# Kernel tuning notes

Measured on AMD Instinct MI355X. Metric: run time of the kernel, lower is better.

The kernel has to match this reference:

```python
import jax, jax.numpy as jnp
import numpy as np
from jax import lax

NUM_HEADS = 4
EPS = 1e-12  # torch F.normalize eps


def _conv1x1(x, w):
    # x: [b, cin, h, w], w: [cout, cin] -> [b, cout, h, w]
    return jnp.einsum('bchw,oc->bohw', x, w)


def _dwconv3x3(x, w):
    # depthwise 3x3, padding=1; w: [C, 1, 3, 3]
    return lax.conv_general_dilated(
        x, w, window_strides=(1, 1), padding='SAME',
        feature_group_count=x.shape[1],
        dimension_numbers=('NCHW', 'OIHW', 'NCHW'))


def _l2norm(x):
    # F.normalize over last dim
    n = jnp.linalg.norm(x, axis=-1, keepdims=True)
    return x / jnp.maximum(n, EPS)


def _mdta(q, k, v, temperature, h, w):
    # q,k,v: [b, C, h, w] -> channel attention per head -> [b, C, h, w]
    b, c, _, _ = q.shape
    ch = c // NUM_HEADS
    def to_heads(t):
        return t.reshape(b, NUM_HEADS, ch, h * w)  # b head c (hw)
    qh, kh, vh = to_heads(q), to_heads(k), to_heads(v)
    qh = _l2norm(qh)
    kh = _l2norm(kh)
    attn = jnp.einsum('bhcn,bhdn->bhcd', qh, kh) * temperature  # [b,head,ch,ch]
    attn = jax.nn.softmax(attn, axis=-1)
    out = jnp.einsum('bhcd,bhdn->bhcn', attn, vh)
    return out.reshape(b, c, h, w)


def setup_inputs() -> dict:
    key = jax.random.key(0)
    ks = jax.random.split(key, 7)
    b, c, h, w = 2, 192, 128, 128
    return {
        'x': jax.random.normal(ks[0], (b, c, h, w), jnp.float32),
        'y': jax.random.normal(ks[1], (b, c, h, w), jnp.float32),
        'qkv_w': jax.random.normal(ks[2], (3 * c, c), jnp.float32) * (1.0 / np.sqrt(c)),
        'dw_w': jax.random.normal(ks[3], (3 * c, 1, 3, 3), jnp.float32) * (1.0 / 3.0),
        'kv_w': jax.random.normal(ks[4], (2 * c, c), jnp.float32) * (1.0 / np.sqrt(c)),
        'proj_w': jax.random.normal(ks[5], (c, c), jnp.float32) * (1.0 / np.sqrt(c)),
        'temperature': jnp.ones((NUM_HEADS, 1, 1), jnp.float32),
    }


def reference(x, y, qkv_w, dw_w, kv_w, proj_w, temperature):
    b, c, h, w = x.shape
    qkv = _dwconv3x3(_conv1x1(x, qkv_w), dw_w)
    q, k, v = jnp.split(qkv, 3, axis=1)
    # intra_fusion_attention(q, y): kv from y, channel attention with q
    kv = _conv1x1(y, kv_w)
    k2, v2 = jnp.split(kv, 2, axis=1)
    q = _mdta(q, k2, v2, temperature, h, w)
    out = _mdta(q, k, v, temperature, h, w)
    return _conv1x1(out, proj_w)
```

## Files before the change

kernel.cpp:

```cpp
#include <hip/hip_runtime.h>
#include <hip/hip_bf16.h>

#define HW 16384
#define IMGW 128
#define Bsz 2
#define Cc 192
#define NH 4
#define CH 48
static const size_t CP = (size_t)Cc * HW;

typedef __attribute__((ext_vector_type(4))) float f32x4;
typedef __attribute__((ext_vector_type(8))) short short8;
typedef __attribute__((ext_vector_type(8))) unsigned short bf16x8;
typedef __attribute__((ext_vector_type(4))) unsigned short bf16x4;

__device__ __forceinline__ unsigned short f2bf(float f) {
  __hip_bfloat16 h = __float2bfloat16(f);
  return *reinterpret_cast<unsigned short*>(&h);
}
__device__ __forceinline__ float bf2f(unsigned short u) {
  union { unsigned int i; float f; } v;
  v.i = (unsigned int)u << 16;
  return v.f;
}

#define NWQKV (576 * 192)
#define NWKV  (384 * 192)
__global__ __launch_bounds__(256) void cast_weights_kernel(
    const float* __restrict__ qkv_w, const float* __restrict__ kv_w,
    unsigned short* __restrict__ wqkv, unsigned short* __restrict__ wkv) {
  int i = blockIdx.x * 256 + threadIdx.x;
  if (i < NWQKV) wqkv[i] = f2bf(qkv_w[i]);
  else if (i < NWQKV + NWKV) wkv[i - NWQKV] = f2bf(kv_w[i - NWQKV]);
}

#define APAD 200

template <int INKIND, int OUTBF16>
__global__ __launch_bounds__(256) void conv_mfma_kernel(
    const void* __restrict__ src, size_t src_bstride,
    const unsigned short* __restrict__ wb, size_t wstride,
    void* __restrict__ outv, int Cout) {
  __shared__ __align__(16) short As[64 * APAD];
  __shared__ __align__(16) short Bs[64 * APAD];
  unsigned int* As32 = (unsigned int*)As;
  const int b = blockIdx.z;
  const int hw0 = blockIdx.x * 64;
  const int tid = threadIdx.x;
  const int lane = tid & 63, wid = tid >> 6;
  const int wm = wid & 1, wn = wid >> 1;
  const int l = tid & 15, pp0 = tid >> 4;
  const unsigned short* wbbase = wb + (size_t)b * wstride;
  const int NT = Cout >> 6;

  #pragma unroll
  for (int kp = 0; kp < 3; ++kp) {
    #pragma unroll
    for (int it = 0; it < 2; ++it) {
      int pp = pp0 + 16 * it;
      int c0 = kp * 64 + 2 * pp;
      if (INKIND == 1) {
        const float* r0 = (const float*)src + (size_t)b * src_bstride +
                          (size_t)c0 * HW + hw0 + l * 4;
        f32x4 v0 = *(const f32x4*)r0;
        f32x4 v1 = *(const f32x4*)(r0 + HW);
        #pragma unroll
        for (int i = 0; i < 4; ++i)
          As32[(l * 4 + i) * (APAD / 2) + kp * 32 + pp] =
              (unsigned int)f2bf(v0[i]) | ((unsigned int)f2bf(v1[i]) << 16);
      } else {
        const unsigned short* r0 = (const unsigned short*)src +
                                   (size_t)b * src_bstride +
                                   (size_t)c0 * HW + hw0 + l * 4;
        bf16x4 v0 = *(const bf16x4*)r0;
        bf16x4 v1 = *(const bf16x4*)(r0 + HW);
        #pragma unroll
        for (int i = 0; i < 4; ++i)
          As32[(l * 4 + i) * (APAD / 2) + kp * 32 + pp] =
              (unsigned int)v0[i] | ((unsigned int)v1[i] << 16);
      }
    }
  }

  for (int ot = 0; ot < NT; ++ot) {
    const unsigned short* wbb = wbbase + (size_t)(ot * 64) * Cc;
    #pragma unroll
    for (int p = 0; p < 6; ++p) {
      int i = tid + p * 256;
      int row = i / 24, cc = i - (i / 24) * 24;
      *(short8*)&Bs[row * APAD + cc * 8] =
          *(const short8*)(wbb + (size_t)row * Cc + cc * 8);
    }
    __syncthreads();
    f32x4 acc[2][2] = {};
    #pragma unroll
    for (int ks = 0; ks < 6; ++ks) {
      short8 bfrag[2];
      #pragma unroll
      for (int fn = 0; fn < 2; ++fn)
        bfrag[fn] = *(short8*)&Bs[(wn * 32 + fn * 16 + (lane & 15)) * APAD +
                                  ks * 32 + (lane >> 4) * 8];
      #pragma unroll
      for (int fm = 0; fm < 2; ++fm) {
        short8 afrag = *(short8*)&As[(wm * 32 + fm * 16 + (lane & 15)) * APAD +
                                     ks * 32 + (lane >> 4) * 8];
        #pragma unroll
        for (int fn = 0; fn < 2; ++fn)
          acc[fm][fn] = __builtin_amdgcn_mfma_f32_16x16x32_bf16(
              afrag, bfrag[fn], acc[fm][fn], 0, 0, 0);
      }
    }
    __syncthreads();
    #pragma unroll
    for (int fm = 0; fm < 2; ++fm)
      #pragma unroll
      for (int fn = 0; fn < 2; ++fn) {
        int o = ot * 64 + wn * 32 + fn * 16 + (lane & 15);
        int hw = hw0 + wm * 32 + fm * 16 + ((lane >> 4) << 2);
        if (OUTBF16) {
          bf16x4 u;
          #pragma unroll
          for (int r = 0; r < 4; ++r) u[r] = f2bf(acc[fm][fn][r]);
          *(bf16x4*)&((unsigned short*)outv)[((size_t)b * Cout + o) * HW + hw] = u;
        } else {
          *(f32x4*)&((float*)outv)[((size_t)b * Cout + o) * HW + hw] = acc[fm][fn];
        }
      }
  }
}

__global__ __launch_bounds__(256) void dwconv_kernel(
    const unsigned short* __restrict__ in, const float* __restrict__ wgt,
    unsigned short* __restrict__ out, int Ctot) {
  const int b = blockIdx.z, ch = blockIdx.y;
  const int p0 = blockIdx.x * 2048 + threadIdx.x * 8;
  const int y = p0 >> 7, x0 = p0 & 127;
  const unsigned short* ip = in + ((size_t)b * Ctot + ch) * HW;
  const float* wp = wgt + ch * 9;
  float acc[8] = {};
  #pragma unroll
  for (int dy = -1; dy <= 1; ++dy) {
    int yy = y + dy;
    if (yy < 0 || yy > IMGW - 1) continue;
    const unsigned short* rp = ip + yy * IMGW;
    float r[10];
    bf16x8 mid = *(const bf16x8*)&rp[x0];
    #pragma unroll
    for (int e = 0; e < 8; ++e) r[e + 1] = bf2f(mid[e]);
    r[0] = (x0 > 0) ? bf2f(rp[x0 - 1]) : 0.f;
    r[9] = (x0 < 120) ? bf2f(rp[x0 + 8]) : 0.f;
    #pragma unroll
    for (int dx = 0; dx < 3; ++dx) {
      float wv = wp[(dy + 1) * 3 + dx];
      #pragma unroll
      for (int e = 0; e < 8; ++e) acc[e] += wv * r[e + dx];
    }
  }
  bf16x8 u;
  #pragma unroll
  for (int e = 0; e < 8; ++e) u[e] = f2bf(acc[e]);
  *(bf16x8*)&out[((size_t)b * Ctot + ch) * HW + p0] = u;
}

#define PK 136
#define NCHUNK 16
__global__ __launch_bounds__(256) void gram_mfma_kernel(
    const unsigned short* __restrict__ qkvb,
    const unsigned short* __restrict__ kvb, float* __restrict__ spart,
    float* __restrict__ spartN) {
  __shared__ __align__(16) char lds_raw[4 * 2304 * 4];
  short* Qs = (short*)lds_raw;
  short* Ks = Qs + 48 * PK;
  float* Rs = (float*)lds_raw;
  const int pair = blockIdx.z;
  const int bh = blockIdx.y, b = bh >> 2, hd = bh & 3;
  const int n0 = blockIdx.x * 1024;
  const int tid = threadIdx.x, lane = tid & 63, wid = tid >> 6;
  const unsigned short *ap, *bp;
  size_t as_, bs_;
  if (pair == 0)      { ap = qkvb;      as_ = 3 * CP; bp = kvb;       bs_ = 2 * CP; }
  else if (pair == 1) { ap = kvb + CP;  as_ = 2 * CP; bp = qkvb + CP; bs_ = 3 * CP; }
  else                { ap = kvb + CP;  as_ = 2 * CP; bp = kvb + CP;  bs_ = 2 * CP; }
  const unsigned short* qb = ap + (size_t)b * as_ + (size_t)(hd * CH) * HW + n0;
  const unsigned short* kb = bp + (size_t)b * bs_ + (size_t)(hd * CH) * HW + n0;
  f32x4 acc[3][3] = {};
  float sqA[3] = {}, sqB[3] = {};
  #pragma unroll 1
  for (int it = 0; it < 8; ++it) {
    #pragma unroll
    for (int p = 0; p < 3; ++p) {
      int c = tid + p * 256;
      int row = c >> 4, col = c & 15;
      short8 vq = *(const short8*)(qb + (size_t)row * HW + it * 128 + col * 8);
      short8 vk = *(const short8*)(kb + (size_t)row * HW + it * 128 + col * 8);
      *(short8*)&Qs[row * PK + col * 8] = vq;
      *(short8*)&Ks[row * PK + col * 8] = vk;
      if (pair == 0) {
        float aq = 0.f, ak = 0.f;
        #pragma unroll
        for (int j = 0; j < 8; ++j) {
          float q = bf2f((unsigned short)vq[j]);
          float k = bf2f((unsigned short)vk[j]);
          aq += q * q;
          ak += k * k;
        }
        sqA[p] += aq;
        sqB[p] += ak;
      } else if (pair == 1) {
        float ak = 0.f;
        #pragma unroll
        for (int j = 0; j < 8; ++j) {
          float k = bf2f((unsigned short)vk[j]);
          ak += k * k;
        }
        sqB[p] += ak;
      }
    }
    __syncthreads();
    short8 af[3], bfr[3];
    #pragma unroll
    for (int t = 0; t < 3; ++t) {
      af[t]  = *(short8*)&Qs[(t * 16 + (lane & 15)) * PK + wid * 32 + (lane >> 4) * 8];
      bfr[t] = *(short8*)&Ks[(t * 16 + (lane & 15)) * PK + wid * 32 + (lane >> 4) * 8];
    }
    #pragma unroll
    for (int mt = 0; mt < 3; ++mt)
      #pragma unroll
      for (int nt = 0; nt < 3; ++nt)
        acc[mt][nt] = __builtin_amdgcn_mfma_f32_16x16x32_bf16(
            af[mt], bfr[nt], acc[mt][nt], 0, 0, 0);
    __syncthreads();
  }
  if (pair < 2) {
    #pragma unroll
    for (int p = 0; p < 3; ++p)
      #pragma unroll
      for (int off = 1; off < 16; off <<= 1) {
        if (pair == 0) sqA[p] += __shfl_xor(sqA[p], off);
        sqB[p] += __shfl_xor(sqB[p], off);
      }
    if ((tid & 15) == 0) {
      int r0 = tid >> 4;
      float* np = spartN + ((size_t)bh * NCHUNK + blockIdx.x) * 144;
      #pragma unroll
      for (int p = 0; p < 3; ++p) {
        if (pair == 0) {
          np[r0 + 16 * p] = sqA[p];
          np[48 + r0 + 16 * p] = sqB[p];
        } else {
          np[96 + r0 + 16 * p] = sqB[p];
        }
      }
    }
  }
  #pragma unroll
  for (int mt = 0; mt < 3; ++mt)
    #pragma unroll
    for (int nt = 0; nt < 3; ++nt)
      #pragma unroll
      for (int r = 0; r < 4; ++r) {
        int i = mt * 16 + ((lane >> 4) << 2) + r;
        int j = nt * 16 + (lane & 15);
        Rs[wid * 2304 + i * 48 + j] = acc[mt][nt][r];
      }
  __syncthreads();
  float* sp = spart + ((size_t)(pair * 8 + bh) * NCHUNK + blockIdx.x) * 2304;
  for (int e = tid; e < 2304; e += 256)
    sp[e] = Rs[e] + Rs[2304 + e] + Rs[2 * 2304 + e] + Rs[3 * 2304 + e];
}

__global__ __launch_bounds__(256) void reduce_kernel(
    const float* __restrict__ spart, const float* __restrict__ spartN,
    float* __restrict__ G, float* __restrict__ inv) {
  int idx = blockIdx.x * 256 + threadIdx.x;
  if (idx < 3 * 8 * 2304) {
    int pb = idx / 2304;
    int e = idx - pb * 2304;
    const float* sp = spart + (size_t)pb * NCHUNK * 2304 + e;
    float s = 0.f;
    #pragma unroll
    for (int c = 0; c < NCHUNK; ++c) s += sp[(size_t)c * 2304];
    G[idx] = s;
  } else if (idx < 3 * 8 * 2304 + 1152) {
    int t = idx - 3 * 8 * 2304;
    int kind = t / 384;
    int row = t - kind * 384;
    int b = row / 192;
    int rr = row - b * 192;
    int hd = rr / 48, r = rr - hd * 48;
    int bh = b * 4 + hd;
    const float* np = spartN + (size_t)bh * NCHUNK * 144 + kind * 48 + r;
    float s = 0.f;
    #pragma unroll
    for (int c = 0; c < NCHUNK; ++c) s += np[c * 144];
    inv[t] = 1.f / fmaxf(sqrtf(s), 1e-12f);
  }
}

__global__ __launch_bounds__(256) void finalize_kernel(
    const float* __restrict__ G, const float* __restrict__ inv,
    const float* __restrict__ temp, const float* __restrict__ proj_w,
    unsigned short* __restrict__ Mb) {
  __shared__ float A1[2304], GVV[2304], GVK[2304], S2[2304];
  __shared__ unsigned short Pb[192 * 48];
  __shared__ float invq1[48];
  const int bh = blockIdx.x, b = bh >> 2, hd = bh & 3;
  const int tid = threadIdx.x;
  const float tp = temp[hd];
  const float* invQ  = inv;
  const float* invK2 = inv + 384;
  const float* invK  = inv + 768;
  for (int e = tid; e < 192 * 48; e += 256) {
    int o = e / 48, i = e - (e / 48) * 48;
    Pb[e] = f2bf(proj_w[(size_t)o * Cc + hd * 48 + i]);
  }
  for (int e = tid; e < 2304; e += 256) {
    int i = e / 48, j = e - i * 48;
    A1[e] = G[(size_t)(0 * 8 + bh) * 2304 + e] *
            invQ[b * Cc + hd * CH + i] * invK2[b * Cc + hd * CH + j] * tp;
    GVV[e] = G[(size_t)(2 * 8 + bh) * 2304 + e];
    GVK[e] = G[(size_t)(1 * 8 + bh) * 2304 + e];
  }
  __syncthreads();
  if (tid < 192) {
    const int i = tid >> 2, g = tid & 3;
    float v[12];
    float m = -1e30f;
    #pragma unroll
    for (int k = 0; k < 12; ++k) {
      v[k] = A1[i * 48 + g * 12 + k];
      m = fmaxf(m, v[k]);
    }
    m = fmaxf(m, __shfl_xor(m, 1));
    m = fmaxf(m, __shfl_xor(m, 2));
    float sum = 0.f;
    #pragma unroll
    for (int k = 0; k < 12; ++k) {
      v[k] = expf(v[k] - m);
      sum += v[k];
    }
    sum += __shfl_xor(sum, 1);
    sum += __shfl_xor(sum, 2);
    float r = 1.f / sum;
    #pragma unroll
    for (int k = 0; k < 12; ++k) A1[i * 48 + g * 12 + k] = v[k] * r;
  }
  __syncthreads();
  const int ti = tid >> 4, tj = tid & 15;
  {
    float c[3][3] = {};
    #pragma unroll 4
    for (int d = 0; d < 48; ++d) {
      float a0 = A1[ti * 48 + d], a1 = A1[(ti + 16) * 48 + d],
            a2 = A1[(ti + 32) * 48 + d];
      float b0 = GVV[d * 48 + tj], b1 = GVV[d * 48 + tj + 16],
            b2 = GVV[d * 48 + tj + 32];
      c[0][0] += a0 * b0; c[0][1] += a0 * b1; c[0][2] += a0 * b2;
      c[1][0] += a1 * b0; c[1][1] += a1 * b1; c[1][2] += a1 * b2;
      c[2][0] += a2 * b0; c[2][1] += a2 * b1; c[2][2] += a2 * b2;
    }
    #pragma unroll
    for (int ii = 0; ii < 3; ++ii) {
      float p = 0.f;
      #pragma unroll
      for (int jj = 0; jj < 3; ++jj)
        p += c[ii][jj] * A1[(ti + 16 * ii) * 48 + tj + 16 * jj];
      p += __shfl_xor(p, 1);
      p += __shfl_xor(p, 2);
      p += __shfl_xor(p, 4);
      p += __shfl_xor(p, 8);
      if (tj == 0)
        invq1[ti + 16 * ii] = 1.f / fmaxf(sqrtf(fmaxf(p, 0.f)), 1e-12f);
    }
  }
  __syncthreads();
  {
    float s[3][3] = {};
    #pragma unroll 4
    for (int d = 0; d < 48; ++d) {
      float a0 = A1[ti * 48 + d], a1 = A1[(ti + 16) * 48 + d],
            a2 = A1[(ti + 32) * 48 + d];
      float b0 = GVK[d * 48 + tj], b1 = GVK[d * 48 + tj + 16],
            b2 = GVK[d * 48 + tj + 32];
      s[0][0] += a0 * b0; s[0][1] += a0 * b1; s[0][2] += a0 * b2;
      s[1][0] += a1 * b0; s[1][1] += a1 * b1; s[1][2] += a1 * b2;
      s[2][0] += a2 * b0; s[2][1] += a2 * b1; s[2][2] += a2 * b2;
    }
    #pragma unroll
    for (int ii = 0; ii < 3; ++ii)
      #pragma unroll
      for (int jj = 0; jj < 3; ++jj) {
        int i = ti + 16 * ii, j = tj + 16 * jj;
        S2[i * 48 + j] = s[ii][jj] * invq1[i] *
                         invK[b * Cc + hd * CH + j] * tp;
      }
  }
  __syncthreads();
  if (tid < 192) {
    const int i = tid >> 2, g = tid & 3;
    float v[12];
    float m = -1e30f;
    #pragma unroll
    for (int k = 0; k < 12; ++k) {
      v[k] = S2[i * 48 + g * 12 + k];
      m = fmaxf(m, v[k]);
    }
    m = fmaxf(m, __shfl_xor(m, 1));
    m = fmaxf(m, __shfl_xor(m, 2));
    float sum = 0.f;
    #pragma unroll
    for (int k = 0; k < 12; ++k) {
      v[k] = expf(v[k] - m);
      sum += v[k];
    }
    sum += __shfl_xor(sum, 1);
    sum += __shfl_xor(sum, 2);
    float r = 1.f / sum;
    #pragma unroll
    for (int k = 0; k < 12; ++k) S2[i * 48 + g * 12 + k] = v[k] * r;
  }
  __syncthreads();
  {
    float macc[12][3] = {};
    #pragma unroll 4
    for (int d = 0; d < 48; ++d) {
      float b0 = S2[d * 48 + tj], b1 = S2[d * 48 + tj + 16],
            b2 = S2[d * 48 + tj + 32];
      #pragma unroll
      for (int rr = 0; rr < 12; ++rr) {
        float a = bf2f(Pb[(rr * 16 + ti) * 48 + d]);
        macc[rr][0] += a * b0;
        macc[rr][1] += a * b1;
        macc[rr][2] += a * b2;
      }
    }
    #pragma unroll
    for (int rr = 0; rr < 12; ++rr)
      #pragma unroll
      for (int cc = 0; cc < 3; ++cc) {
        int o = rr * 16 + ti, j = tj + 16 * cc;
        Mb[((size_t)b * Cc + o) * Cc + hd * 48 + j] = f2bf(macc[rr][cc]);
      }
  }
}

extern "C" void kernel_launch(void* const* d_in, const int* in_sizes, int n_in,
                              void* d_out, int out_size, void* d_ws, size_t ws_size,
                              hipStream_t stream) {
  const float* x      = (const float*)d_in[0];
  const float* y      = (const float*)d_in[1];
  const float* qkv_w  = (const float*)d_in[2];
  const float* dw_w   = (const float*)d_in[3];
  const float* kv_w   = (const float*)d_in[4];
  const float* proj_w = (const float*)d_in[5];
  const float* temp   = (const float*)d_in[6];
  float* out = (float*)d_out;
  float* ws  = (float*)d_ws;

  const size_t SF = (size_t)Bsz * CP;
  unsigned short* qkvb   = (unsigned short*)ws;
  unsigned short* kvb    = (unsigned short*)(ws + 3 * SF / 2);
  unsigned short* qkvpre = (unsigned short*)(ws + 5 * SF / 2);
  float* inv    = ws + 4 * SF;
  float* spart  = inv + 1152;
  float* spartN = spart + (size_t)3 * 8 * NCHUNK * 2304;
  float* G      = spartN + (size_t)8 * NCHUNK * 144;
  unsigned short* Mb   = (unsigned short*)(G + 3 * 8 * 2304);
  unsigned short* wqkv = Mb + (size_t)Bsz * Cc * Cc;
  unsigned short* wkv  = wqkv + NWQKV;

  dim3 blk(256);

  cast_weights_kernel<<<dim3((NWQKV + NWKV + 255) / 256), blk, 0, stream>>>(
      qkv_w, kv_w, wqkv, wkv);

  conv_mfma_kernel<1, 1><<<dim3(HW / 64, 1, Bsz), blk, 0, stream>>>(
      x, CP, wqkv, 0, qkvpre, 3 * Cc);
  dwconv_kernel<<<dim3(HW / 2048, 3 * Cc, Bsz), blk, 0, stream>>>(
      qkvpre, dw_w, qkvb, 3 * Cc);
  conv_mfma_kernel<1, 1><<<dim3(HW / 64, 1, Bsz), blk, 0, stream>>>(
      y, CP, wkv, 0, kvb, 2 * Cc);

  gram_mfma_kernel<<<dim3(NCHUNK, 8, 3), blk, 0, stream>>>(
      qkvb, kvb, spart, spartN);
  reduce_kernel<<<dim3((3 * 8 * 2304 + 1152 + 255) / 256), blk, 0, stream>>>(
      spart, spartN, G, inv);

  finalize_kernel<<<dim3(8), blk, 0, stream>>>(G, inv, temp, proj_w, Mb);

  conv_mfma_kernel<2, 0><<<dim3(HW / 64, 1, Bsz), blk, 0, stream>>>(
      qkvb + 2 * CP, 3 * CP, Mb, (size_t)Cc * Cc, out, Cc);
}
```

Baseline: 119.8 us.

## Fuse depthwise conv into gram and projection kernels, merge front convs

Removes the standalone depthwise 3x3 pass and recomputes the depthwise conv on the fly inside the gram kernel (for q and k) and inside the final projection GEMM's A-tile load (for v). The two front 1x1 convs become one launch, and the weight bf16 cast is folded into the B-tile loads, which drops the separate cast kernel. The aim is to avoid writing and re-reading the full qkv intermediate and to cut kernel launches. In exchange, the stencil is computed redundantly with extra halo loads, weights are re-converted per block, and a 3x9-float weight array adds register pressure in the gram kernel.

```diff
diff --git a/kernel.cpp b/kernel.cpp
--- a/kernel.cpp
+++ b/kernel.cpp
@@ -24,34 +24,80 @@
   return v.f;
 }
 
-#define NWQKV (576 * 192)
-#define NWKV  (384 * 192)
-__global__ __launch_bounds__(256) void cast_weights_kernel(
+__device__ __forceinline__ short8 dw3x3_row8(
+    const unsigned short* __restrict__ chimg, int yrow, int x0,
+    const float* __restrict__ w9) {
+  float acc[8] = {};
+  #pragma unroll
+  for (int dy = -1; dy <= 1; ++dy) {
+    int yy = yrow + dy;
+    if (yy >= 0 && yy <= IMGW - 1) {
+      const unsigned short* rp = chimg + yy * IMGW;
+      float r[10];
+      bf16x8 mid = *(const bf16x8*)&rp[x0];
+      #pragma unroll
+      for (int e = 0; e < 8; ++e) r[e + 1] = bf2f(mid[e]);
+      r[0] = (x0 > 0) ? bf2f(rp[x0 - 1]) : 0.f;
+      r[9] = (x0 < 120) ? bf2f(rp[x0 + 8]) : 0.f;
+      #pragma unroll
+      for (int dx = 0; dx < 3; ++dx) {
+        float wv = w9[(dy + 1) * 3 + dx];
+        #pragma unroll
+        for (int e = 0; e < 8; ++e) acc[e] += wv * r[e + dx];
+      }
+    }
+  }
+  short8 o;
+  #pragma unroll
+  for (int e = 0; e < 8; ++e) o[e] = (short)f2bf(acc[e]);
+  return o;
+}
+
+__device__ __forceinline__ void dw3x3_row4(
+    const unsigned short* __restrict__ chimg, const float* __restrict__ w9,
+    int yrow, int xb, float* __restrict__ acc) {
+  acc[0] = acc[1] = acc[2] = acc[3] = 0.f;
+  #pragma unroll
+  for (int dy = -1; dy <= 1; ++dy) {
+    int yy = yrow + dy;
+    if (yy >= 0 && yy <= IMGW - 1) {
+      const unsigned short* rp = chimg + yy * IMGW;
+      float r[6];
+      bf16x4 mid = *(const bf16x4*)&rp[xb];
+      #pragma unroll
+      for (int i = 0; i < 4; ++i) r[i + 1] = bf2f(mid[i]);
+      r[0] = (xb > 0) ? bf2f(rp[xb - 1]) : 0.f;
+      r[5] = (xb < 124) ? bf2f(rp[xb + 4]) : 0.f;
+      #pragma unroll
+      for (int dx = 0; dx < 3; ++dx) {
+        float wv = w9[(dy + 1) * 3 + dx];
+        #pragma unroll
+        for (int i = 0; i < 4; ++i) acc[i] += wv * r[i + dx];
+      }
+    }
+  }
+}
+
+#define APAD 200
+
+__global__ __launch_bounds__(256) void conv_front_kernel(
+    const float* __restrict__ xin, const float* __restrict__ yin,
     const float* __restrict__ qkv_w, const float* __restrict__ kv_w,
-    unsigned short* __restrict__ wqkv, unsigned short* __restrict__ wkv) {
-  int i = blockIdx.x * 256 + threadIdx.x;
-  if (i < NWQKV) wqkv[i] = f2bf(qkv_w[i]);
-  else if (i < NWQKV + NWKV) wkv[i - NWQKV] = f2bf(kv_w[i - NWQKV]);
-}
-
-#define APAD 200
-
-template <int INKIND, int OUTBF16>
-__global__ __launch_bounds__(256) void conv_mfma_kernel(
-    const void* __restrict__ src, size_t src_bstride,
-    const unsigned short* __restrict__ wb, size_t wstride,
-    void* __restrict__ outv, int Cout) {
+    unsigned short* __restrict__ qkvpre, unsigned short* __restrict__ kvb) {
   __shared__ __align__(16) short As[64 * APAD];
   __shared__ __align__(16) short Bs[64 * APAD];
   unsigned int* As32 = (unsigned int*)As;
-  const int b = blockIdx.z;
+  const int z = blockIdx.z, isKV = z >> 1, b = z & 1;
+  const float* src = isKV ? yin : xin;
+  const float* wsrc = isKV ? kv_w : qkv_w;
+  unsigned short* dst = isKV ? kvb : qkvpre;
+  const int Cout = isKV ? 2 * Cc : 3 * Cc;
+  const int NT = Cout >> 6;
   const int hw0 = blockIdx.x * 64;
   const int tid = threadIdx.x;
   const int lane = tid & 63, wid = tid >> 6;
   const int wm = wid & 1, wn = wid >> 1;
   const int l = tid & 15, pp0 = tid >> 4;
-  const unsigned short* wbbase = wb + (size_t)b * wstride;
-  const int NT = Cout >> 6;
 
   #pragma unroll
   for (int kp = 0; kp < 3; ++kp) {
@@ -59,37 +105,32 @@
     for (int it = 0; it < 2; ++it) {
       int pp = pp0 + 16 * it;
       int c0 = kp * 64 + 2 * pp;
-      if (INKIND == 1) {
-        const float* r0 = (const float*)src + (size_t)b * src_bstride +
-                          (size_t)c0 * HW + hw0 + l * 4;
-        f32x4 v0 = *(const f32x4*)r0;
-        f32x4 v1 = *(const f32x4*)(r0 + HW);
-        #pragma unroll
-        for (int i = 0; i < 4; ++i)
-          As32[(l * 4 + i) * (APAD / 2) + kp * 32 + pp] =
-              (unsigned int)f2bf(v0[i]) | ((unsigned int)f2bf(v1[i]) << 16);
-      } else {
-        const unsigned short* r0 = (const unsigned short*)src +
-                                   (size_t)b * src_bstride +
-                                   (size_t)c0 * HW + hw0 + l * 4;
-        bf16x4 v0 = *(const bf16x4*)r0;
-        bf16x4 v1 = *(const bf16x4*)(r0 + HW);
-        #pragma unroll
-        for (int i = 0; i < 4; ++i)
-          As32[(l * 4 + i) * (APAD / 2) + kp * 32 + pp] =
-              (unsigned int)v0[i] | ((unsigned int)v1[i] << 16);
-      }
+      const float* r0 = src + (size_t)b * CP + (size_t)c0 * HW + hw0 + l * 4;
+      f32x4 v0 = *(const f32x4*)r0;
+      f32x4 v1 = *(const f32x4*)(r0 + HW);
+      #pragma unroll
+      for (int i = 0; i < 4; ++i)
+        As32[(l * 4 + i) * (APAD / 2) + kp * 32 + pp] =
+            (unsigned int)f2bf(v0[i]) | ((unsigned int)f2bf(v1[i]) << 16);
     }
   }
 
   for (int ot = 0; ot < NT; ++ot) {
-    const unsigned short* wbb = wbbase + (size_t)(ot * 64) * Cc;
+    const float* wbb = wsrc + (size_t)(ot * 64) * Cc;
     #pragma unroll
     for (int p = 0; p < 6; ++p) {
       int i = tid + p * 256;
       int row = i / 24, cc = i - (i / 24) * 24;
-      *(short8*)&Bs[row * APAD + cc * 8] =
-          *(const short8*)(wbb + (size_t)row * Cc + cc * 8);
+      const float* wr = wbb + (size_t)row * Cc + cc * 8;
+      f32x4 w0 = *(const f32x4*)wr;
+      f32x4 w1 = *(const f32x4*)(wr + 4);
+      short8 v;
+      #pragma unroll
+      for (int j = 0; j < 4; ++j) {
+        v[j] = (short)f2bf(w0[j]);
+        v[j + 4] = (short)f2bf(w1[j]);
+      }
+      *(short8*)&Bs[row * APAD + cc * 8] = v;
     }
     __syncthreads();
     f32x4 acc[2][2] = {};
@@ -117,90 +158,88 @@
       for (int fn = 0; fn < 2; ++fn) {
         int o = ot * 64 + wn * 32 + fn * 16 + (lane & 15);
         int hw = hw0 + wm * 32 + fm * 16 + ((lane >> 4) << 2);
-        if (OUTBF16) {
-          bf16x4 u;
-          #pragma unroll
-          for (int r = 0; r < 4; ++r) u[r] = f2bf(acc[fm][fn][r]);
-          *(bf16x4*)&((unsigned short*)outv)[((size_t)b * Cout + o) * HW + hw] = u;
-        } else {
-          *(f32x4*)&((float*)outv)[((size_t)b * Cout + o) * HW + hw] = acc[fm][fn];
-        }
-      }
-  }
-}
-
-__global__ __launch_bounds__(256) void dwconv_kernel(
-    const unsigned short* __restrict__ in, const float* __restrict__ wgt,
-    unsigned short* __restrict__ out, int Ctot) {
-  const int b = blockIdx.z, ch = blockIdx.y;
-  const int p0 = blockIdx.x * 2048 + threadIdx.x * 8;
-  const int y = p0 >> 7, x0 = p0 & 127;
-  const unsigned short* ip = in + ((size_t)b * Ctot + ch) * HW;
-  const float* wp = wgt + ch * 9;
-  float acc[8] = {};
-  #pragma unroll
-  for (int dy = -1; dy <= 1; ++dy) {
-    int yy = y + dy;
-    if (yy < 0 || yy > IMGW - 1) continue;
-    const unsigned short* rp = ip + yy * IMGW;
-    float r[10];
-    bf16x8 mid = *(const bf16x8*)&rp[x0];
-    #pragma unroll
-    for (int e = 0; e < 8; ++e) r[e + 1] = bf2f(mid[e]);
-    r[0] = (x0 > 0) ? bf2f(rp[x0 - 1]) : 0.f;
-    r[9] = (x0 < 120) ? bf2f(rp[x0 + 8]) : 0.f;
-    #pragma unroll
-    for (int dx = 0; dx < 3; ++dx) {
-      float wv = wp[(dy + 1) * 3 + dx];
-      #pragma unroll
-      for (int e = 0; e < 8; ++e) acc[e] += wv * r[e + dx];
-    }
-  }
-  bf16x8 u;
-  #pragma unroll
-  for (int e = 0; e < 8; ++e) u[e] = f2bf(acc[e]);
-  *(bf16x8*)&out[((size_t)b * Ctot + ch) * HW + p0] = u;
+        bf16x4 u;
+        #pragma unroll
+        for (int r = 0; r < 4; ++r) u[r] = f2bf(acc[fm][fn][r]);
+        *(bf16x4*)&dst[((size_t)b * Cout + o) * HW + hw] = u;
+      }
+  }
 }
 
 #define PK 136
 #define NCHUNK 16
 __global__ __launch_bounds__(256) void gram_mfma_kernel(
-    const unsigned short* __restrict__ qkvb,
-    const unsigned short* __restrict__ kvb, float* __restrict__ spart,
-    float* __restrict__ spartN) {
+    const unsigned short* __restrict__ qkvpre,
+    const unsigned short* __restrict__ kvb,
+    const float* __restrict__ dw_w,
+    float* __restrict__ spart, float* __restrict__ spartN) {
   __shared__ __align__(16) char lds_raw[4 * 2304 * 4];
   short* Qs = (short*)lds_raw;
   short* Ks = Qs + 48 * PK;
   float* Rs = (float*)lds_raw;
   const int pair = blockIdx.z;
   const int bh = blockIdx.y, b = bh >> 2, hd = bh & 3;
-  const int n0 = blockIdx.x * 1024;
+  const int chunk = blockIdx.x;
+  const int n0 = chunk * 1024;
   const int tid = threadIdx.x, lane = tid & 63, wid = tid >> 6;
-  const unsigned short *ap, *bp;
-  size_t as_, bs_;
-  if (pair == 0)      { ap = qkvb;      as_ = 3 * CP; bp = kvb;       bs_ = 2 * CP; }
-  else if (pair == 1) { ap = kvb + CP;  as_ = 2 * CP; bp = qkvb + CP; bs_ = 3 * CP; }
-  else                { ap = kvb + CP;  as_ = 2 * CP; bp = kvb + CP;  bs_ = 2 * CP; }
-  const unsigned short* qb = ap + (size_t)b * as_ + (size_t)(hd * CH) * HW + n0;
-  const unsigned short* kb = bp + (size_t)b * bs_ + (size_t)(hd * CH) * HW + n0;
+  const unsigned short* plainA = nullptr;
+  const unsigned short* plainB = nullptr;
+  const unsigned short* stA = nullptr;
+  const unsigned short* stB = nullptr;
+  const float* sW = nullptr;
+  if (pair == 0) {
+    stA = qkvpre + (size_t)b * 3 * CP;
+    sW = dw_w;
+    plainB = kvb + (size_t)b * 2 * CP;
+  } else if (pair == 1) {
+    plainA = kvb + (size_t)b * 2 * CP + CP;
+    stB = qkvpre + (size_t)b * 3 * CP + CP;
+    sW = dw_w + 192 * 9;
+  } else {
+    plainA = kvb + (size_t)b * 2 * CP + CP;
+    plainB = plainA;
+  }
+  int rowp[3];
+  #pragma unroll
+  for (int p = 0; p < 3; ++p) rowp[p] = (tid + p * 256) >> 4;
+  const int colx = (tid & 15) * 8;
+  float w9[3][9];
+  if (pair < 2) {
+    #pragma unroll
+    for (int p = 0; p < 3; ++p) {
+      const float* wp = sW + (size_t)(hd * CH + rowp[p]) * 9;
+      #pragma unroll
+      for (int k = 0; k < 9; ++k) w9[p][k] = wp[k];
+    }
+  }
   f32x4 acc[3][3] = {};
   float sqA[3] = {}, sqB[3] = {};
   #pragma unroll 1
   for (int it = 0; it < 8; ++it) {
+    const int yrow = chunk * 8 + it;
     #pragma unroll
     for (int p = 0; p < 3; ++p) {
-      int c = tid + p * 256;
-      int row = c >> 4, col = c & 15;
-      short8 vq = *(const short8*)(qb + (size_t)row * HW + it * 128 + col * 8);
-      short8 vk = *(const short8*)(kb + (size_t)row * HW + it * 128 + col * 8);
-      *(short8*)&Qs[row * PK + col * 8] = vq;
-      *(short8*)&Ks[row * PK + col * 8] = vk;
+      int row = rowp[p];
+      size_t choff = (size_t)(hd * CH + row) * HW;
+      short8 va, vb;
+      if (pair == 0) {
+        va = dw3x3_row8(stA + choff, yrow, colx, w9[p]);
+        vb = *(const short8*)(plainB + choff + n0 + it * 128 + colx);
+      } else if (pair == 1) {
+        va = *(const short8*)(plainA + choff + n0 + it * 128 + colx);
+        vb = dw3x3_row8(stB + choff, yrow, colx, w9[p]);
+      } else {
+        va = *(const short8*)(plainA + choff + n0 + it * 128 + colx);
+        vb = va;
+      }
+      *(short8*)&Qs[row * PK + colx] = va;
+      *(short8*)&Ks[row * PK + colx] = vb;
       if (pair == 0) {
         float aq = 0.f, ak = 0.f;
         #pragma unroll
         for (int j = 0; j < 8; ++j) {
-          float q = bf2f((unsigned short)vq[j]);
-          float k = bf2f((unsigned short)vk[j]);
+          float q = bf2f((unsigned short)va[j]);
+          float k = bf2f((unsigned short)vb[j]);
           aq += q * q;
           ak += k * k;
         }
@@ -210,7 +249,7 @@
         float ak = 0.f;
         #pragma unroll
         for (int j = 0; j < 8; ++j) {
-          float k = bf2f((unsigned short)vk[j]);
+          float k = bf2f((unsigned short)vb[j]);
           ak += k * k;
         }
         sqB[p] += ak;
@@ -241,7 +280,7 @@
       }
     if ((tid & 15) == 0) {
       int r0 = tid >> 4;
-      float* np = spartN + ((size_t)bh * NCHUNK + blockIdx.x) * 144;
+      float* np = spartN + ((size_t)bh * NCHUNK + chunk) * 144;
       #pragma unroll
       for (int p = 0; p < 3; ++p) {
         if (pair == 0) {
@@ -264,7 +303,7 @@
         Rs[wid * 2304 + i * 48 + j] = acc[mt][nt][r];
       }
   __syncthreads();
-  float* sp = spart + ((size_t)(pair * 8 + bh) * NCHUNK + blockIdx.x) * 2304;
+  float* sp = spart + ((size_t)(pair * 8 + bh) * NCHUNK + chunk) * 2304;
   for (int e = tid; e < 2304; e += 256)
     sp[e] = Rs[e] + Rs[2304 + e] + Rs[2 * 2304 + e] + Rs[3 * 2304 + e];
 }
@@ -444,6 +483,81 @@
   }
 }
 
+__global__ __launch_bounds__(256) void conv_back_kernel(
+    const unsigned short* __restrict__ qkvpre, const float* __restrict__ dw_w,
+    const unsigned short* __restrict__ Mb, float* __restrict__ out) {
+  __shared__ __align__(16) short As[64 * APAD];
+  __shared__ __align__(16) short Bs[64 * APAD];
+  unsigned int* As32 = (unsigned int*)As;
+  const int b = blockIdx.z;
+  const int hw0 = blockIdx.x * 64;
+  const int tid = threadIdx.x;
+  const int lane = tid & 63, wid = tid >> 6;
+  const int wm = wid & 1, wn = wid >> 1;
+  const int l = tid & 15, pp0 = tid >> 4;
+  const unsigned short* vbase = qkvpre + (size_t)b * 3 * CP + 2 * CP;
+  const float* dwv = dw_w + 384 * 9;
+  const unsigned short* wbbase = Mb + (size_t)b * Cc * Cc;
+  const int yimg = hw0 >> 7;
+  const int xb = (hw0 & 127) + l * 4;
+
+  #pragma unroll
+  for (int kp = 0; kp < 3; ++kp) {
+    #pragma unroll
+    for (int it = 0; it < 2; ++it) {
+      int pp = pp0 + 16 * it;
+      int c0 = kp * 64 + 2 * pp;
+      float a0[4], a1[4];
+      dw3x3_row4(vbase + (size_t)c0 * HW, dwv + (size_t)c0 * 9, yimg, xb, a0);
+      dw3x3_row4(vbase + (size_t)(c0 + 1) * HW, dwv + (size_t)(c0 + 1) * 9,
+                 yimg, xb, a1);
+      #pragma unroll
+      for (int i = 0; i < 4; ++i)
+        As32[(l * 4 + i) * (APAD / 2) + kp * 32 + pp] =
+            (unsigned int)f2bf(a0[i]) | ((unsigned int)f2bf(a1[i]) << 16);
+    }
+  }
+
+  for (int ot = 0; ot < 3; ++ot) {
+    const unsigned short* wbb = wbbase + (size_t)(ot * 64) * Cc;
+    #pragma unroll
+    for (int p = 0; p < 6; ++p) {
+      int i = tid + p * 256;
+      int row = i / 24, cc = i - (i / 24) * 24;
+      *(short8*)&Bs[row * APAD + cc * 8] =
+          *(const short8*)(wbb + (size_t)row * Cc + cc * 8);
+    }
+    __syncthreads();
+    f32x4 acc[2][2] = {};
+    #pragma unroll
+    for (int ks = 0; ks < 6; ++ks) {
+      short8 bfrag[2];
+      #pragma unroll
+      for (int fn = 0; fn < 2; ++fn)
+        bfrag[fn] = *(short8*)&Bs[(wn * 32 + fn * 16 + (lane & 15)) * APAD +
+                                  ks * 32 + (lane >> 4) * 8];
+      #pragma unroll
+      for (int fm = 0; fm < 2; ++fm) {
+        short8 afrag = *(short8*)&As[(wm * 32 + fm * 16 + (lane & 15)) * APAD +
+                                     ks * 32 + (lane >> 4) * 8];
+        #pragma unroll
+        for (int fn = 0; fn < 2; ++fn)
+          acc[fm][fn] = __builtin_amdgcn_mfma_f32_16x16x32_bf16(
+              afrag, bfrag[fn], acc[fm][fn], 0, 0, 0);
+      }
+    }
+    __syncthreads();
+    #pragma unroll
+    for (int fm = 0; fm < 2; ++fm)
+      #pragma unroll
+      for (int fn = 0; fn < 2; ++fn) {
+        int o = ot * 64 + wn * 32 + fn * 16 + (lane & 15);
+        int hw = hw0 + wm * 32 + fm * 16 + ((lane >> 4) << 2);
+        *(f32x4*)&out[((size_t)b * Cc + o) * HW + hw] = acc[fm][fn];
+      }
+  }
+}
+
 extern "C" void kernel_launch(void* const* d_in, const int* in_sizes, int n_in,
                               void* d_out, int out_size, void* d_ws, size_t ws_size,
                               hipStream_t stream) {
@@ -458,36 +572,27 @@
   float* ws  = (float*)d_ws;
 
   const size_t SF = (size_t)Bsz * CP;
-  unsigned short* qkvb   = (unsigned short*)ws;
+  unsigned short* qkvpre = (unsigned short*)ws;
   unsigned short* kvb    = (unsigned short*)(ws + 3 * SF / 2);
-  unsigned short* qkvpre = (unsigned short*)(ws + 5 * SF / 2);
-  float* inv    = ws + 4 * SF;
+  float* inv    = ws + 5 * SF / 2;
   float* spart  = inv + 1152;
   float* spartN = spart + (size_t)3 * 8 * NCHUNK * 2304;
   float* G      = spartN + (size_t)8 * NCHUNK * 144;
-  unsigned short* Mb   = (unsigned short*)(G + 3 * 8 * 2304);
-  unsigned short* wqkv = Mb + (size_t)Bsz * Cc * Cc;
-  unsigned short* wkv  = wqkv + NWQKV;
+  unsigned short* Mb = (unsigned short*)(G + 3 * 8 * 2304);
 
   dim3 blk(256);
 
-  cast_weights_kernel<<<dim3((NWQKV + NWKV + 255) / 256), blk, 0, stream>>>(
-      qkv_w, kv_w, wqkv, wkv);
-
-  conv_mfma_kernel<1, 1><<<dim3(HW / 64, 1, Bsz), blk, 0, stream>>>(
-      x, CP, wqkv, 0, qkvpre, 3 * Cc);
-  dwconv_kernel<<<dim3(HW / 2048, 3 * Cc, Bsz), blk, 0, stream>>>(
-      qkvpre, dw_w, qkvb, 3 * Cc);
-  conv_mfma_kernel<1, 1><<<dim3(HW / 64, 1, Bsz), blk, 0, stream>>>(
-      y, CP, wkv, 0, kvb, 2 * Cc);
+  conv_front_kernel<<<dim3(HW / 64, 1, 2 * Bsz), blk, 0, stream>>>(
+      x, y, qkv_w, kv_w, qkvpre, kvb);
 
   gram_mfma_kernel<<<dim3(NCHUNK, 8, 3), blk, 0, stream>>>(
-      qkvb, kvb, spart, spartN);
+      qkvpre, kvb, dw_w, spart, spartN);
+
   reduce_kernel<<<dim3((3 * 8 * 2304 + 1152 + 255) / 256), blk, 0, stream>>>(
       spart, spartN, G, inv);
 
   finalize_kernel<<<dim3(8), blk, 0, stream>>>(G, inv, temp, proj_w, Mb);
 
-  conv_mfma_kernel<2, 0><<<dim3(HW / 64, 1, Bsz), blk, 0, stream>>>(
-      qkvb + 2 * CP, 3 * CP, Mb, (size_t)Cc * Cc, out, Cc);
-}
+  conv_back_kernel<<<dim3(HW / 64, 1, Bsz), blk, 0, stream>>>(
+      qkvpre, dw_w, Mb, out);
+}
```

Result: slower. 149.1 us (+24.4%).
